# Optimization experiments

Hardware: AMD Instinct MI355X
Metric: run time of the kernel (lower is better)

Reference implementation:

```python
import math
import jax, jax.numpy as jnp
import numpy as np

N_LAYERS = 6
N_HEADS = 8
WINDOW = 4
LN_EPS = 1e-6


def _get_rel_emb(emb, length):
    # emb: [1, 2*WINDOW+1, kc] -> [1, 2*length-1, kc]
    max_rel = 2 * WINDOW + 1
    pad = max(0, length - (WINDOW + 1))
    start = max(0, WINDOW + 1 - length)
    end = max_rel + 2 * length - 1
    if pad > 0:
        emb = jnp.pad(emb, ((0, 0), (pad, pad), (0, 0)))
    return emb[:, start:end]


def _rel_to_abs(x):
    # x: [b,h,l,2l-1] -> [b,h,l,l]
    b, h, l, _ = x.shape
    x = jnp.pad(x, ((0, 0), (0, 0), (0, 0), (0, 1)))
    xf = x.reshape(b, h, l * 2 * l)
    xf = jnp.pad(xf, ((0, 0), (0, 0), (0, l - 1)))
    return xf.reshape(b, h, l + 1, 2 * l - 1)[:, :, :l, l - 1:]


def _abs_to_rel(x):
    # x: [b,h,l,l] -> [b,h,l,2l-1]
    b, h, l, _ = x.shape
    x = jnp.pad(x, ((0, 0), (0, 0), (0, 0), (0, l - 1)))
    xf = x.reshape(b, h, -1)
    xf = jnp.pad(xf, ((0, 0), (0, 0), (l, 0)))
    return xf.reshape(b, h, l, 2 * l)[..., 1:]


def _layer_norm(x, scale, bias):
    m = jnp.mean(x, axis=-1, keepdims=True)
    v = jnp.mean(jnp.square(x - m), axis=-1, keepdims=True)
    return (x - m) * jax.lax.rsqrt(v + LN_EPS) * scale + bias


def _forward(x, x_mask, Wq, bq, Wk, bk, Wv, bv, Wo, bo, emb_rel_k, emb_rel_v,
             ln1_scale, ln1_bias, W1, b1, W2, b2, ln2_scale, ln2_bias):
    B, T, C = x.shape
    H = N_HEADS
    KC = C // H
    scale = 1.0 / math.sqrt(KC)
    attn_mask = x_mask[:, :, None, :] * x_mask[:, :, :, None]  # [B,1,T,T]
    mask_t = jnp.transpose(x_mask, (0, 2, 1))  # [B,T,1]
    x = x * mask_t
    for l in range(N_LAYERS):
        # --- relative-position multi-head self-attention ---
        q = (x @ Wq[l] + bq[l]).reshape(B, T, H, KC).transpose(0, 2, 1, 3)
        k = (x @ Wk[l] + bk[l]).reshape(B, T, H, KC).transpose(0, 2, 1, 3)
        v = (x @ Wv[l] + bv[l]).reshape(B, T, H, KC).transpose(0, 2, 1, 3)
        scores = jnp.einsum('bhqd,bhkd->bhqk', q * scale, k)
        rk = _get_rel_emb(emb_rel_k[l], T)[0]  # [2T-1, KC] (heads shared)
        rel_logits = jnp.einsum('bhld,md->bhlm', q * scale, rk)
        scores = scores + _rel_to_abs(rel_logits)
        scores = jnp.where(attn_mask == 0, -10000.0, scores)
        p = jax.nn.softmax(scores, axis=-1)
        out = jnp.einsum('bhqk,bhkd->bhqd', p, v)
        rv = _get_rel_emb(emb_rel_v[l], T)[0]
        out = out + jnp.einsum('bhlm,md->bhld', _abs_to_rel(p), rv)
        out = out.transpose(0, 2, 1, 3).reshape(B, T, C)
        y = out @ Wo[l] + bo[l]
        x = _layer_norm(x + y, ln1_scale[l], ln1_bias[l])
        # --- pointwise conv FFN (kernel_size=1) ---
        h1 = jax.nn.relu((x * mask_t) @ W1[l] + b1[l])
        y = (h1 * mask_t) @ W2[l] + b2[l]
        y = y * mask_t
        x = _layer_norm(x + y, ln2_scale[l], ln2_bias[l])
    return x * mask_t


def setup_inputs() -> dict:
    key = jax.random.key(0)
    B, T, C, F, L, H = 8, 768, 512, 2048, N_LAYERS, N_HEADS
    KC = C // H
    ks = jax.random.split(key, 10)
    nrm = lambda k, s, sd=0.02: jax.random.normal(k, s, jnp.float32) * sd
    return {
        'x': jax.random.normal(ks[0], (B, T, C), jnp.float32),
        'x_mask': jnp.ones((B, 1, T), jnp.float32),
        'Wq': nrm(ks[1], (L, C, C)), 'bq': jnp.zeros((L, C), jnp.float32),
        'Wk': nrm(ks[2], (L, C, C)), 'bk': jnp.zeros((L, C), jnp.float32),
        'Wv': nrm(ks[3], (L, C, C)), 'bv': jnp.zeros((L, C), jnp.float32),
        'Wo': nrm(ks[4], (L, C, C)), 'bo': jnp.zeros((L, C), jnp.float32),
        'emb_rel_k': nrm(ks[5], (L, 1, 2 * WINDOW + 1, KC), KC ** -0.5),
        'emb_rel_v': nrm(ks[6], (L, 1, 2 * WINDOW + 1, KC), KC ** -0.5),
        'ln1_scale': jnp.ones((L, C), jnp.float32), 'ln1_bias': jnp.zeros((L, C), jnp.float32),
        'W1': nrm(ks[7], (L, C, F)), 'b1': jnp.zeros((L, F), jnp.float32),
        'W2': nrm(ks[8], (L, F, C)), 'b2': jnp.zeros((L, C), jnp.float32),
        'ln2_scale': jnp.ones((L, C), jnp.float32), 'ln2_bias': jnp.zeros((L, C), jnp.float32),
    }


def reference(x, x_mask, Wq, bq, Wk, bk, Wv, bv, Wo, bo, emb_rel_k, emb_rel_v,
              ln1_scale, ln1_bias, W1, b1, W2, b2, ln2_scale, ln2_bias):
    return _forward(x, x_mask, Wq, bq, Wk, bk, Wv, bv, Wo, bo, emb_rel_k, emb_rel_v,
                    ln1_scale, ln1_bias, W1, b1, W2, b2, ln2_scale, ln2_bias)
```

## Files before the change

kernel.cpp:

```cpp
#include <hip/hip_runtime.h>
#include <stdint.h>


typedef unsigned short u16;
typedef __attribute__((ext_vector_type(8))) __bf16 bf16x8;
typedef __attribute__((ext_vector_type(4))) float f32x4;

#define B_ 8
#define T_ 768
#define C_ 512
#define F_ 2048

__device__ __forceinline__ float b2f(u16 u) {
    union { float f; uint32_t i; } x; x.i = ((uint32_t)u) << 16; return x.f;
}
__device__ __forceinline__ u16 f2b(float f) {
    union { float f; uint32_t i; } x; x.f = f;
    return (u16)((x.i + 0x7fffu + ((x.i >> 16) & 1u)) >> 16);
}

template <int EPI>
__global__ __launch_bounds__(256) void gemm_bt4(
    const u16* __restrict__ A, int aStride,
    const u16* __restrict__ Bt, int bStride,
    const float* __restrict__ bias,
    u16* __restrict__ out, int oStride, int K, float epiScale)
{
    const int tid = threadIdx.x;
    const int wave = tid >> 6, lane = tid & 63;
    const int wm = wave & 1, wn = wave >> 1;
    const int quad = lane >> 4, l16 = lane & 15;
    const int m0 = blockIdx.x * 64;
    const int n0 = blockIdx.y * 64;

    __shared__ u16 As[64 * 64];
    __shared__ u16 Bs[64 * 64];

    const f32x4 vzero = {0.f, 0.f, 0.f, 0.f};
    f32x4 acc[2][2];
#pragma unroll
    for (int i = 0; i < 2; ++i)
#pragma unroll
        for (int j = 0; j < 2; ++j) acc[i][j] = vzero;

    for (int k0 = 0; k0 < K; k0 += 64) {
#pragma unroll
        for (int i = 0; i < 2; ++i) {
            int c = tid + i * 256;
            int row = c >> 3, pc = c & 7, lc = pc ^ (row & 7);
            *(uint4*)&As[c * 8] =
                *(const uint4*)(A + (long long)(m0 + row) * aStride + (k0 + lc * 8));
            *(uint4*)&Bs[c * 8] =
                *(const uint4*)(Bt + (long long)(n0 + row) * bStride + (k0 + lc * 8));
        }
        __syncthreads();
        __builtin_amdgcn_s_setprio(1);
#pragma unroll
        for (int ks = 0; ks < 2; ++ks) {
            bf16x8 af[2], bfr[2];
#pragma unroll
            for (int mi = 0; mi < 2; ++mi) {
                int row = wm * 32 + mi * 16 + l16;
                int pc = ((ks << 2) | quad) ^ (row & 7);
                af[mi] = *(const bf16x8*)&As[row * 64 + pc * 8];
            }
#pragma unroll
            for (int ni = 0; ni < 2; ++ni) {
                int row = wn * 32 + ni * 16 + l16;
                int pc = ((ks << 2) | quad) ^ (row & 7);
                bfr[ni] = *(const bf16x8*)&Bs[row * 64 + pc * 8];
            }
#pragma unroll
            for (int mi = 0; mi < 2; ++mi)
#pragma unroll
                for (int ni = 0; ni < 2; ++ni)
                    acc[mi][ni] = __builtin_amdgcn_mfma_f32_16x16x32_bf16(
                        bfr[ni], af[mi], acc[mi][ni], 0, 0, 0);
        }
        __builtin_amdgcn_s_setprio(0);
        __syncthreads();
    }

#pragma unroll
    for (int mi = 0; mi < 2; ++mi) {
        int row = m0 + wm * 32 + mi * 16 + l16;
#pragma unroll
        for (int ni = 0; ni < 2; ++ni) {
            int colb = n0 + wn * 32 + ni * 16 + quad * 4;
            u16 pk[4];
#pragma unroll
            for (int r = 0; r < 4; ++r) {
                float v = acc[mi][ni][r] + bias[colb + r];
                if (EPI == 1) v = v > 0.f ? v : 0.f;
                if (EPI == 3) { if (colb + r < 512) v *= epiScale; }
                pk[r] = f2b(v);
            }
            uint2 p;
            p.x = (uint32_t)pk[0] | ((uint32_t)pk[1] << 16);
            p.y = (uint32_t)pk[2] | ((uint32_t)pk[3] << 16);
            *(uint2*)(out + (long long)row * oStride + colb) = p;
        }
    }
}

__global__ __launch_bounds__(256) void bandg_k(
    const u16* __restrict__ qkv, const float* __restrict__ erk,
    float* __restrict__ bandg)
{
    __shared__ float erkS[576];
    const int tid = threadIdx.x;
    for (int idx = tid; idx < 576; idx += 256) erkS[idx] = erk[idx];
    __syncthreads();
    const int gid = blockIdx.x * 256 + tid;
    const int row = gid >> 3, h = gid & 7;
    const u16* q = qkv + (long long)row * 1536 + h * 64;
    float acc[9];
#pragma unroll
    for (int e = 0; e < 9; ++e) acc[e] = 0.f;
#pragma unroll
    for (int c = 0; c < 8; ++c) {
        uint4 d4 = *(const uint4*)(q + c * 8);
        const uint32_t dw[4] = {d4.x, d4.y, d4.z, d4.w};
#pragma unroll
        for (int j = 0; j < 8; ++j) {
            u16 uu = (u16)((dw[j >> 1] >> ((j & 1) * 16)) & 0xffff);
            float qv = b2f(uu);
            int d = c * 8 + j;
#pragma unroll
            for (int e = 0; e < 9; ++e) acc[e] += qv * erkS[e * 64 + d];
        }
    }
    float* o = bandg + (long long)gid * 9;
#pragma unroll
    for (int e = 0; e < 9; ++e) o[e] = acc[e];
}

__global__ __launch_bounds__(256) void flash_attn(
    const u16* __restrict__ qkv, const u16* __restrict__ vt,
    const float* __restrict__ mask, const float* __restrict__ bandg,
    const float* __restrict__ erv, u16* __restrict__ outb)
{
    const int tid = threadIdx.x;
    const int w = tid >> 6, lane = tid & 63;
    const int quad = lane >> 4, l16 = lane & 15;
    const int orig = blockIdx.y * 12 + blockIdx.x;
    const int swz = (orig & 7) * 96 + (orig >> 3);
    const int qt = swz % 12, bh = swz / 12;
    const int b = bh >> 3, h = bh & 7;
    const int q0 = qt * 64;

    __shared__ u16 Ql[64 * 64];
    __shared__ u16 Kt[2][64 * 64];
    __shared__ u16 Vt[2][64 * 64];
    __shared__ u16 Pl[4][16 * 64];
    __shared__ float bandk[64][10];
    __shared__ float maskK[2][64];

#pragma unroll
    for (int i = 0; i < 2; ++i) {
        int c = tid + i * 256;
        int r = c >> 3, pc = c & 7, lc = pc ^ (r & 7);
        *(uint4*)&Ql[c * 8] =
            *(const uint4*)(qkv + (long long)(b * T_ + q0 + r) * 1536 + h * 64 + lc * 8);
    }
#pragma unroll
    for (int i = 0; i < 2; ++i) {
        int c = tid + i * 256;
        int r = c >> 3, pc = c & 7, lc = pc ^ (r & 7);
        *(uint4*)&Kt[0][c * 8] =
            *(const uint4*)(qkv + (long long)(b * T_ + r) * 1536 + 512 + h * 64 + lc * 8);
        *(uint4*)&Vt[0][c * 8] =
            *(const uint4*)(vt + ((long long)bh * 64 + r) * T_ + lc * 8);
    }
    if (tid < 64) maskK[0][tid] = mask[b * T_ + tid];
    for (int idx = tid; idx < 576; idx += 256) {
        int r = idx / 9, e = idx - r * 9;
        bandk[r][e] = bandg[((long long)(b * T_ + q0 + r) * 8 + h) * 9 + e];
    }

    const int i_row = q0 + w * 16 + l16;
    const float mi = mask[b * T_ + i_row];
    float m_run = -1e30f, l_run = 0.f;
    const f32x4 vzero = {0.f, 0.f, 0.f, 0.f};
    f32x4 vacc[4] = {vzero, vzero, vzero, vzero};
    float pb[3] = {0.f, 0.f, 0.f};

    __syncthreads();
    bf16x8 qf[2];
#pragma unroll
    for (int ks = 0; ks < 2; ++ks) {
        int r = w * 16 + l16;
        int pc = ((ks << 2) | quad) ^ (r & 7);
        qf[ks] = *(const bf16x8*)&Ql[r * 64 + pc * 8];
    }

    int cbuf = 0;
    for (int kt = 0; kt < 12; ++kt) {
        uint4 kreg[2], vreg[2];
        float mreg = 0.f;
        const bool pre = (kt < 11);
        if (pre) {
            const int ktn = kt + 1;
#pragma unroll
            for (int i = 0; i < 2; ++i) {
                int c = tid + i * 256;
                int r = c >> 3, pc = c & 7, lc = pc ^ (r & 7);
                kreg[i] = *(const uint4*)(qkv + (long long)(b * T_ + ktn * 64 + r) * 1536
                                          + 512 + h * 64 + lc * 8);
                vreg[i] = *(const uint4*)(vt + ((long long)bh * 64 + r) * T_
                                          + ktn * 64 + lc * 8);
            }
            if (tid < 64) mreg = mask[b * T_ + ktn * 64 + tid];
        }

        const float mkv = maskK[cbuf][lane];
        const bool tile_clean = (__ballot(mkv == 0.f) == 0ull);
        const bool fast = tile_clean && (mi != 0.f);
        const bool has_band = (kt * 64 <= q0 + w * 16 + 19) &&
                              (kt * 64 + 67 >= q0 + w * 16);

        f32x4 sacc[4];
#pragma unroll
        for (int ni = 0; ni < 4; ++ni) sacc[ni] = vzero;
        __builtin_amdgcn_s_setprio(1);
#pragma unroll
        for (int ks = 0; ks < 2; ++ks)
#pragma unroll
            for (int ni = 0; ni < 4; ++ni) {
                int r = ni * 16 + l16;
                int pc = ((ks << 2) | quad) ^ (r & 7);
                bf16x8 kf = *(const bf16x8*)&Kt[cbuf][r * 64 + pc * 8];
                sacc[ni] = __builtin_amdgcn_mfma_f32_16x16x32_bf16(kf, qf[ks], sacc[ni], 0, 0, 0);
            }
        __builtin_amdgcn_s_setprio(0);

        if (has_band) {
#pragma unroll
            for (int ni = 0; ni < 4; ++ni)
#pragma unroll
                for (int r = 0; r < 4; ++r) {
                    int jl = ni * 16 + quad * 4 + r;
                    int dlt = kt * 64 + jl - i_row;
                    if (dlt >= -4 && dlt <= 4)
                        sacc[ni][r] += bandk[w * 16 + l16][dlt + 4];
                }
        }
        if (!fast) {
#pragma unroll
            for (int ni = 0; ni < 4; ++ni)
#pragma unroll
                for (int r = 0; r < 4; ++r) {
                    int jl = ni * 16 + quad * 4 + r;
                    if (mi * maskK[cbuf][jl] == 0.f) sacc[ni][r] = -10000.0f;
                }
        }

        float mx = -1e30f;
#pragma unroll
        for (int ni = 0; ni < 4; ++ni)
#pragma unroll
            for (int r = 0; r < 4; ++r) mx = fmaxf(mx, sacc[ni][r]);
        mx = fmaxf(mx, __shfl_xor(mx, 16));
        mx = fmaxf(mx, __shfl_xor(mx, 32));
        float m_new = fmaxf(m_run, mx);
        float alpha = __expf(m_run - m_new);
        m_run = m_new;
        l_run *= alpha;
#pragma unroll
        for (int ni = 0; ni < 4; ++ni) vacc[ni] = vacc[ni] * alpha;
#pragma unroll
        for (int k = 0; k < 3; ++k) pb[k] *= alpha;

        float lsum = 0.f;
#pragma unroll
        for (int ni = 0; ni < 4; ++ni) {
            u16 pk[4];
#pragma unroll
            for (int r = 0; r < 4; ++r) {
                float u = __expf(sacc[ni][r] - m_new);
                lsum += u;
                pk[r] = f2b(u);
            }
            int c0 = ni * 16 + quad * 4;
            int phys = (((c0 >> 3) ^ (l16 & 7)) << 3) + (c0 & 7);
            uint2 p;
            p.x = (uint32_t)pk[0] | ((uint32_t)pk[1] << 16);
            p.y = (uint32_t)pk[2] | ((uint32_t)pk[3] << 16);
            *(uint2*)&Pl[w][l16 * 64 + phys] = p;
        }
        l_run += lsum;

        if (has_band) {
#pragma unroll
            for (int k = 0; k < 3; ++k) {
                int e = quad * 3 + k;
                if (e < 9) {
                    int jl = i_row + e - 4 - kt * 64;
                    if (jl >= 0 && jl < 64) {
                        int phys = (((jl >> 3) ^ (l16 & 7)) << 3) + (jl & 7);
                        pb[k] += b2f(Pl[w][l16 * 64 + phys]);
                    }
                }
            }
        }

        __builtin_amdgcn_s_setprio(1);
#pragma unroll
        for (int ks = 0; ks < 2; ++ks) {
            int pcc = ((ks << 2) | quad) ^ (l16 & 7);
            bf16x8 pf = *(const bf16x8*)&Pl[w][l16 * 64 + pcc * 8];
#pragma unroll
            for (int ni = 0; ni < 4; ++ni) {
                int r = ni * 16 + l16;
                int pc = ((ks << 2) | quad) ^ (r & 7);
                bf16x8 vf = *(const bf16x8*)&Vt[cbuf][r * 64 + pc * 8];
                vacc[ni] = __builtin_amdgcn_mfma_f32_16x16x32_bf16(vf, pf, vacc[ni], 0, 0, 0);
            }
        }
        __builtin_amdgcn_s_setprio(0);

        if (pre) {
#pragma unroll
            for (int i = 0; i < 2; ++i) {
                int c = tid + i * 256;
                *(uint4*)&Kt[cbuf ^ 1][c * 8] = kreg[i];
                *(uint4*)&Vt[cbuf ^ 1][c * 8] = vreg[i];
            }
            if (tid < 64) maskK[cbuf ^ 1][tid] = mreg;
            __syncthreads();
            cbuf ^= 1;
        }
    }

    l_run += __shfl_xor(l_run, 16);
    l_run += __shfl_xor(l_run, 32);
    const float rinv = 1.f / l_run;

    float pband[9];
#pragma unroll
    for (int e = 0; e < 9; ++e) {
        float val = (quad == e / 3) ? pb[e % 3] : 0.f;
        val += __shfl_xor(val, 16);
        val += __shfl_xor(val, 32);
        pband[e] = val * rinv;
    }

    u16* orow = outb + (long long)(b * T_ + i_row) * C_ + h * 64;
#pragma unroll
    for (int ni = 0; ni < 4; ++ni) {
        u16 pk[4];
#pragma unroll
        for (int r = 0; r < 4; ++r) {
            int d = ni * 16 + quad * 4 + r;
            float v = vacc[ni][r] * rinv;
#pragma unroll
            for (int e = 0; e < 9; ++e) v += pband[e] * erv[e * 64 + d];
            pk[r] = f2b(v);
        }
        uint2 p;
        p.x = (uint32_t)pk[0] | ((uint32_t)pk[1] << 16);
        p.y = (uint32_t)pk[2] | ((uint32_t)pk[3] << 16);
        *(uint2*)(orow + ni * 16 + quad * 4) = p;
    }
}

__global__ void transpose_qkvo(const float* __restrict__ Wq, const float* __restrict__ Wk,
                               const float* __restrict__ Wv, const float* __restrict__ Wo,
                               u16* __restrict__ wqkvT, u16* __restrict__ woT)
{
    __shared__ u16 tile[32][33];
    const int z = blockIdx.z, l = z >> 2, which = z & 3;
    const float* src = (which == 0 ? Wq : which == 1 ? Wk : which == 2 ? Wv : Wo)
                       + (long long)l * 262144;
    u16* dst = (which == 3) ? woT + (long long)l * 262144
                            : wqkvT + (long long)l * 786432 + which * 262144;
    const int r0 = blockIdx.y * 32, c0 = blockIdx.x * 32;
    const int tx = threadIdx.x, ty = threadIdx.y;
#pragma unroll
    for (int i = 0; i < 32; i += 8)
        tile[ty + i][tx] = f2b(src[(long long)(r0 + ty + i) * 512 + (c0 + tx)]);
    __syncthreads();
#pragma unroll
    for (int i = 0; i < 32; i += 8)
        dst[(long long)(c0 + ty + i) * 512 + (r0 + tx)] = tile[tx][ty + i];
}

__global__ void transpose_f2bL(const float* __restrict__ src0, int sStride, long long sLayer,
                               u16* __restrict__ dst0, int dStride, long long dLayer)
{
    __shared__ u16 tile[32][33];
    const int l = blockIdx.z;
    const float* src = src0 + (long long)l * sLayer;
    u16* dst = dst0 + (long long)l * dLayer;
    const int r0 = blockIdx.y * 32, c0 = blockIdx.x * 32;
    const int tx = threadIdx.x, ty = threadIdx.y;
#pragma unroll
    for (int i = 0; i < 32; i += 8)
        tile[ty + i][tx] = f2b(src[(long long)(r0 + ty + i) * sStride + (c0 + tx)]);
    __syncthreads();
#pragma unroll
    for (int i = 0; i < 32; i += 8)
        dst[(long long)(c0 + ty + i) * dStride + (r0 + tx)] = tile[tx][ty + i];
}

__global__ void transpose_b(const u16* __restrict__ src, long long sB1, long long sB2, int sStride,
                            u16* __restrict__ dst, long long dB1, long long dB2, int dStride)
{
    __shared__ u16 tile[32][33];
    const int z = blockIdx.z, zb = z >> 3, zh = z & 7;
    src += (long long)zb * sB1 + (long long)zh * sB2;
    dst += (long long)zb * dB1 + (long long)zh * dB2;
    const int r0 = blockIdx.y * 32, c0 = blockIdx.x * 32;
    const int tx = threadIdx.x, ty = threadIdx.y;
#pragma unroll
    for (int i = 0; i < 32; i += 8)
        tile[ty + i][tx] = src[(long long)(r0 + ty + i) * sStride + (c0 + tx)];
    __syncthreads();
#pragma unroll
    for (int i = 0; i < 32; i += 8)
        dst[(long long)(c0 + ty + i) * dStride + (r0 + tx)] = tile[tx][ty + i];
}

__global__ void concat_bias(const float* __restrict__ bq, const float* __restrict__ bk,
                            const float* __restrict__ bv, float* __restrict__ dst)
{
    int i = blockIdx.x * 256 + threadIdx.x;
    int l = i / 1536, n = i - l * 1536;
    float v = (n < 512) ? bq[l * 512 + n]
             : (n < 1024 ? bk[l * 512 + (n - 512)] : bv[l * 512 + (n - 1024)]);
    dst[i] = v;
}

__global__ void mask_in(const float* __restrict__ x, const float* __restrict__ mask,
                        u16* __restrict__ out)
{
    int i4 = (blockIdx.x * 256 + threadIdx.x) * 4;
    float4 xv = *(const float4*)(x + i4);
    float m = mask[i4 >> 9];
    u16 pk[4] = {f2b(xv.x * m), f2b(xv.y * m), f2b(xv.z * m), f2b(xv.w * m)};
    uint2 p; p.x = (uint32_t)pk[0] | ((uint32_t)pk[1] << 16);
    p.y = (uint32_t)pk[2] | ((uint32_t)pk[3] << 16);
    *(uint2*)(out + i4) = p;
}

__global__ void mask_out(const u16* __restrict__ x, const float* __restrict__ mask,
                         float* __restrict__ out)
{
    int i4 = (blockIdx.x * 256 + threadIdx.x) * 4;
    uint2 p = *(const uint2*)(x + i4);
    float m = mask[i4 >> 9];
    float4 o;
    o.x = b2f((u16)(p.x & 0xffff)) * m;
    o.y = b2f((u16)(p.x >> 16)) * m;
    o.z = b2f((u16)(p.y & 0xffff)) * m;
    o.w = b2f((u16)(p.y >> 16)) * m;
    *(float4*)(out + i4) = o;
}

__global__ __launch_bounds__(256) void add_ln(
    const u16* __restrict__ x, const u16* __restrict__ y,
    const float* __restrict__ sc, const float* __restrict__ bi,
    u16* __restrict__ outx)
{
    const int wave = threadIdx.x >> 6, lane = threadIdx.x & 63;
    const long long r = (long long)blockIdx.x * 4 + wave;
    const u16* xr = x + r * C_;
    const u16* yr = y + r * C_;
    float v[8], s = 0.f;
#pragma unroll
    for (int it = 0; it < 2; ++it) {
        int j0 = it * 256 + lane * 4;
        uint2 px = *(const uint2*)(xr + j0);
        uint2 py = *(const uint2*)(yr + j0);
        v[it * 4 + 0] = b2f((u16)(px.x & 0xffff)) + b2f((u16)(py.x & 0xffff));
        v[it * 4 + 1] = b2f((u16)(px.x >> 16))    + b2f((u16)(py.x >> 16));
        v[it * 4 + 2] = b2f((u16)(px.y & 0xffff)) + b2f((u16)(py.y & 0xffff));
        v[it * 4 + 3] = b2f((u16)(px.y >> 16))    + b2f((u16)(py.y >> 16));
        s += v[it * 4 + 0] + v[it * 4 + 1] + v[it * 4 + 2] + v[it * 4 + 3];
    }
#pragma unroll
    for (int off = 32; off > 0; off >>= 1) s += __shfl_down(s, off);
    s = __shfl(s, 0);
    const float mean = s * (1.f / 512.f);
    float var = 0.f;
#pragma unroll
    for (int l = 0; l < 8; ++l) { float d = v[l] - mean; var += d * d; }
#pragma unroll
    for (int off = 32; off > 0; off >>= 1) var += __shfl_down(var, off);
    var = __shfl(var, 0);
    const float rs = rsqrtf(var * (1.f / 512.f) + 1e-6f);
    u16* orow = outx + r * C_;
#pragma unroll
    for (int it = 0; it < 2; ++it) {
        int j0 = it * 256 + lane * 4;
        float4 s4 = *(const float4*)(sc + j0);
        float4 b4 = *(const float4*)(bi + j0);
        u16 pk[4];
        pk[0] = f2b((v[it * 4 + 0] - mean) * rs * s4.x + b4.x);
        pk[1] = f2b((v[it * 4 + 1] - mean) * rs * s4.y + b4.y);
        pk[2] = f2b((v[it * 4 + 2] - mean) * rs * s4.z + b4.z);
        pk[3] = f2b((v[it * 4 + 3] - mean) * rs * s4.w + b4.w);
        uint2 p; p.x = (uint32_t)pk[0] | ((uint32_t)pk[1] << 16);
        p.y = (uint32_t)pk[2] | ((uint32_t)pk[3] << 16);
        *(uint2*)(orow + j0) = p;
    }
}

extern "C" void kernel_launch(void* const* d_in, const int* in_sizes, int n_in,
                              void* d_out, int out_size, void* d_ws, size_t ws_size,
                              hipStream_t stream)
{
    const float* x    = (const float*)d_in[0];
    const float* mask = (const float*)d_in[1];
    const float* Wq   = (const float*)d_in[2];
    const float* bq   = (const float*)d_in[3];
    const float* Wk   = (const float*)d_in[4];
    const float* bk   = (const float*)d_in[5];
    const float* Wv   = (const float*)d_in[6];
    const float* bv   = (const float*)d_in[7];
    const float* Wo   = (const float*)d_in[8];
    const float* bo   = (const float*)d_in[9];
    const float* erk  = (const float*)d_in[10];
    const float* erv  = (const float*)d_in[11];
    const float* ln1s = (const float*)d_in[12];
    const float* ln1b = (const float*)d_in[13];
    const float* W1   = (const float*)d_in[14];
    const float* b1   = (const float*)d_in[15];
    const float* W2   = (const float*)d_in[16];
    const float* b2   = (const float*)d_in[17];
    const float* ln2s = (const float*)d_in[18];
    const float* ln2b = (const float*)d_in[19];
    float* out = (float*)d_out;
    u16* ws  = (u16*)d_ws;

    const long long CF = 512LL * 2048;
    const int M = B_ * T_;

    u16* wqkvT   = ws;
    u16* woT     = ws + 4718592;
    u16* w1T     = ws + 6291456;
    u16* w2T     = ws + 12582912;
    float* bqkv  = (float*)(ws + 18874368);
    u16* xb      = ws + 18892800;
    u16* qkvb    = ws + 22038528;
    u16* vtb     = ws + 31475712;
    u16* attnb   = ws + 34621440;
    u16* scr     = ws + 37767168;
    float* bandg = (float*)(ws + 50350080);
    u16* yb      = vtb;

    const dim3 tb(32, 8);

    transpose_qkvo<<<dim3(16, 16, 24), tb, 0, stream>>>(Wq, Wk, Wv, Wo, wqkvT, woT);
    transpose_f2bL<<<dim3(64, 16, 6), tb, 0, stream>>>(W1, 2048, CF, w1T, 512, 1048576);
    transpose_f2bL<<<dim3(16, 64, 6), tb, 0, stream>>>(W2, 512,  CF, w2T, 2048, 1048576);
    concat_bias<<<36, 256, 0, stream>>>(bq, bk, bv, bqkv);
    mask_in<<<(M * 512) / 1024, 256, 0, stream>>>(x, mask, xb);

    for (int l = 0; l < 6; ++l) {
        gemm_bt4<3><<<dim3(96, 24), 256, 0, stream>>>(
            xb, 512, wqkvT + (long long)l * 786432, 512, bqkv + l * 1536,
            qkvb, 1536, 512, 0.125f);
        bandg_k<<<192, 256, 0, stream>>>(qkvb, erk + l * 576, bandg);
        transpose_b<<<dim3(2, 24, 64), tb, 0, stream>>>(
            qkvb + 1024, 768LL * 1536, 64, 1536,
            vtb, 8LL * 64 * 768, 64LL * 768, 768);
        flash_attn<<<dim3(12, 64), 256, 0, stream>>>(
            qkvb, vtb, mask, bandg, erv + l * 576, attnb);
        gemm_bt4<0><<<dim3(96, 8), 256, 0, stream>>>(
            attnb, 512, woT + (long long)l * 262144, 512, bo + l * 512,
            yb, 512, 512, 0.f);
        add_ln<<<1536, 256, 0, stream>>>(xb, yb, ln1s + l * 512, ln1b + l * 512, xb);
        gemm_bt4<1><<<dim3(96, 32), 256, 0, stream>>>(
            xb, 512, w1T + (long long)l * 1048576, 512, b1 + l * 2048,
            scr, 2048, 512, 0.f);
        gemm_bt4<0><<<dim3(96, 8), 256, 0, stream>>>(
            scr, 2048, w2T + (long long)l * 1048576, 2048, b2 + l * 512,
            yb, 512, 2048, 0.f);
        add_ln<<<1536, 256, 0, stream>>>(xb, yb, ln2s + l * 512, ln2b + l * 512, xb);
    }

    mask_out<<<(M * 512) / 1024, 256, 0, stream>>>(xb, mask, out);
}
```

Measured before the change: 998.1 us.

## Double-buffer GEMM tiles and switch flash-attention softmax to exp2 with lazy rescaling

```diff
diff --git a/kernel.cpp b/kernel.cpp
--- a/kernel.cpp
+++ b/kernel.cpp
@@ -10,6 +10,7 @@
 #define T_ 768
 #define C_ 512
 #define F_ 2048
+#define LOG2E 1.4426950408889634f
 
 __device__ __forceinline__ float b2f(u16 u) {
     union { float f; uint32_t i; } x; x.i = ((uint32_t)u) << 16; return x.f;
@@ -20,7 +21,7 @@
 }
 
 template <int EPI>
-__global__ __launch_bounds__(256) void gemm_bt4(
+__global__ __launch_bounds__(256, 4) void gemm_bt4(
     const u16* __restrict__ A, int aStride,
     const u16* __restrict__ Bt, int bStride,
     const float* __restrict__ bias,
@@ -33,8 +34,8 @@
     const int m0 = blockIdx.x * 64;
     const int n0 = blockIdx.y * 64;
 
-    __shared__ u16 As[64 * 64];
-    __shared__ u16 Bs[64 * 64];
+    __shared__ u16 As[2][64 * 64];
+    __shared__ u16 Bs[2][64 * 64];
 
     const f32x4 vzero = {0.f, 0.f, 0.f, 0.f};
     f32x4 acc[2][2];
@@ -43,17 +44,32 @@
 #pragma unroll
         for (int j = 0; j < 2; ++j) acc[i][j] = vzero;
 
+#pragma unroll
+    for (int i = 0; i < 2; ++i) {
+        int c = tid + i * 256;
+        int row = c >> 3, pc = c & 7, lc = pc ^ (row & 7);
+        *(uint4*)&As[0][c * 8] =
+            *(const uint4*)(A + (long long)(m0 + row) * aStride + lc * 8);
+        *(uint4*)&Bs[0][c * 8] =
+            *(const uint4*)(Bt + (long long)(n0 + row) * bStride + lc * 8);
+    }
+    __syncthreads();
+
+    int cb = 0;
     for (int k0 = 0; k0 < K; k0 += 64) {
-#pragma unroll
-        for (int i = 0; i < 2; ++i) {
-            int c = tid + i * 256;
-            int row = c >> 3, pc = c & 7, lc = pc ^ (row & 7);
-            *(uint4*)&As[c * 8] =
-                *(const uint4*)(A + (long long)(m0 + row) * aStride + (k0 + lc * 8));
-            *(uint4*)&Bs[c * 8] =
-                *(const uint4*)(Bt + (long long)(n0 + row) * bStride + (k0 + lc * 8));
-        }
-        __syncthreads();
+        uint4 areg[2], breg[2];
+        const bool pre = (k0 + 64 < K);
+        if (pre) {
+#pragma unroll
+            for (int i = 0; i < 2; ++i) {
+                int c = tid + i * 256;
+                int row = c >> 3, pc = c & 7, lc = pc ^ (row & 7);
+                areg[i] = *(const uint4*)(A + (long long)(m0 + row) * aStride
+                                          + (k0 + 64 + lc * 8));
+                breg[i] = *(const uint4*)(Bt + (long long)(n0 + row) * bStride
+                                          + (k0 + 64 + lc * 8));
+            }
+        }
         __builtin_amdgcn_s_setprio(1);
 #pragma unroll
         for (int ks = 0; ks < 2; ++ks) {
@@ -62,13 +78,13 @@
             for (int mi = 0; mi < 2; ++mi) {
                 int row = wm * 32 + mi * 16 + l16;
                 int pc = ((ks << 2) | quad) ^ (row & 7);
-                af[mi] = *(const bf16x8*)&As[row * 64 + pc * 8];
+                af[mi] = *(const bf16x8*)&As[cb][row * 64 + pc * 8];
             }
 #pragma unroll
             for (int ni = 0; ni < 2; ++ni) {
                 int row = wn * 32 + ni * 16 + l16;
                 int pc = ((ks << 2) | quad) ^ (row & 7);
-                bfr[ni] = *(const bf16x8*)&Bs[row * 64 + pc * 8];
+                bfr[ni] = *(const bf16x8*)&Bs[cb][row * 64 + pc * 8];
             }
 #pragma unroll
             for (int mi = 0; mi < 2; ++mi)
@@ -78,7 +94,16 @@
                         bfr[ni], af[mi], acc[mi][ni], 0, 0, 0);
         }
         __builtin_amdgcn_s_setprio(0);
-        __syncthreads();
+        if (pre) {
+#pragma unroll
+            for (int i = 0; i < 2; ++i) {
+                int c = tid + i * 256;
+                *(uint4*)&As[cb ^ 1][c * 8] = areg[i];
+                *(uint4*)&Bs[cb ^ 1][c * 8] = breg[i];
+            }
+            __syncthreads();
+            cb ^= 1;
+        }
     }
 
 #pragma unroll
@@ -251,41 +276,47 @@
 #pragma unroll
                 for (int r = 0; r < 4; ++r) {
                     int jl = ni * 16 + quad * 4 + r;
-                    if (mi * maskK[cbuf][jl] == 0.f) sacc[ni][r] = -10000.0f;
+                    if (mi * maskK[cbuf][jl] == 0.f) sacc[ni][r] = -14427.0f;
                 }
         }
 
-        float mx = -1e30f;
-#pragma unroll
-        for (int ni = 0; ni < 4; ++ni)
-#pragma unroll
-            for (int r = 0; r < 4; ++r) mx = fmaxf(mx, sacc[ni][r]);
+        float t0, t1, mx;
+        {
+            float a0 = fmaxf(sacc[0][0], sacc[0][1]), a1 = fmaxf(sacc[0][2], sacc[0][3]);
+            float b0 = fmaxf(sacc[1][0], sacc[1][1]), b1 = fmaxf(sacc[1][2], sacc[1][3]);
+            float c0 = fmaxf(sacc[2][0], sacc[2][1]), c1 = fmaxf(sacc[2][2], sacc[2][3]);
+            float d0 = fmaxf(sacc[3][0], sacc[3][1]), d1 = fmaxf(sacc[3][2], sacc[3][3]);
+            t0 = fmaxf(fmaxf(a0, a1), fmaxf(b0, b1));
+            t1 = fmaxf(fmaxf(c0, c1), fmaxf(d0, d1));
+            mx = fmaxf(t0, t1);
+        }
         mx = fmaxf(mx, __shfl_xor(mx, 16));
         mx = fmaxf(mx, __shfl_xor(mx, 32));
         float m_new = fmaxf(m_run, mx);
-        float alpha = __expf(m_run - m_new);
+        if (__any(mx > m_run)) {
+            float alpha = exp2f(m_run - m_new);
+            l_run *= alpha;
+#pragma unroll
+            for (int ni = 0; ni < 4; ++ni) vacc[ni] = vacc[ni] * alpha;
+#pragma unroll
+            for (int k = 0; k < 3; ++k) pb[k] *= alpha;
+        }
         m_run = m_new;
-        l_run *= alpha;
-#pragma unroll
-        for (int ni = 0; ni < 4; ++ni) vacc[ni] = vacc[ni] * alpha;
-#pragma unroll
-        for (int k = 0; k < 3; ++k) pb[k] *= alpha;
 
         float lsum = 0.f;
 #pragma unroll
         for (int ni = 0; ni < 4; ++ni) {
-            u16 pk[4];
-#pragma unroll
-            for (int r = 0; r < 4; ++r) {
-                float u = __expf(sacc[ni][r] - m_new);
-                lsum += u;
-                pk[r] = f2b(u);
-            }
+            float u0 = exp2f(sacc[ni][0] - m_new);
+            float u1 = exp2f(sacc[ni][1] - m_new);
+            float u2 = exp2f(sacc[ni][2] - m_new);
+            float u3 = exp2f(sacc[ni][3] - m_new);
+            lsum += (u0 + u1) + (u2 + u3);
+            union { __bf16 h[2]; uint32_t u; } cA, cB;
+            cA.h[0] = (__bf16)u0; cA.h[1] = (__bf16)u1;
+            cB.h[0] = (__bf16)u2; cB.h[1] = (__bf16)u3;
             int c0 = ni * 16 + quad * 4;
             int phys = (((c0 >> 3) ^ (l16 & 7)) << 3) + (c0 & 7);
-            uint2 p;
-            p.x = (uint32_t)pk[0] | ((uint32_t)pk[1] << 16);
-            p.y = (uint32_t)pk[2] | ((uint32_t)pk[3] << 16);
+            uint2 p; p.x = cA.u; p.y = cB.u;
             *(uint2*)&Pl[w][l16 * 64 + phys] = p;
         }
         l_run += lsum;
@@ -560,7 +591,7 @@
     for (int l = 0; l < 6; ++l) {
         gemm_bt4<3><<<dim3(96, 24), 256, 0, stream>>>(
             xb, 512, wqkvT + (long long)l * 786432, 512, bqkv + l * 1536,
-            qkvb, 1536, 512, 0.125f);
+            qkvb, 1536, 512, 0.125f * LOG2E);
         bandg_k<<<192, 256, 0, stream>>>(qkvb, erk + l * 576, bandg);
         transpose_b<<<dim3(2, 24, 64), tb, 0, stream>>>(
             qkvb + 1024, 768LL * 1536, 64, 1536,
```

Result: slower. 2.401 ms (+140.6%).
